# Kernel optimization log

Hardware: AMD Instinct MI355X
Metric: run time of the kernel (lower is better)

The kernel has to match this reference:

```python
import jax, jax.numpy as jnp
import numpy as np

N_NODES = 50000
N_GRAPHS = 250
NODES_PER_GRAPH = 200
EDGES_PER_GRAPH = 3200  # avg degree 16
F_IN = 128
EMB = 128
HID = 128
VOCAB = 1000
N_REL = 8


def setup_inputs() -> dict:
    key = jax.random.key(0)
    ks = jax.random.split(key, 16)

    # message: col 0 = discrete token id (stored as float), col 1 = continuous value
    disc = jax.random.randint(ks[0], (N_GRAPHS,), 0, VOCAB).astype(jnp.float32)
    cont = jax.random.normal(ks[1], (N_GRAPHS,), dtype=jnp.float32)
    message = jnp.stack([disc, cont], axis=1)  # [B, 2]

    x = jax.random.normal(ks[2], (N_NODES, F_IN), dtype=jnp.float32)

    # within-graph edges: local indices + per-graph node offset
    offs = (jnp.arange(N_GRAPHS, dtype=jnp.int64) * NODES_PER_GRAPH)[:, None]
    src = (jax.random.randint(ks[3], (N_GRAPHS, EDGES_PER_GRAPH), 0, NODES_PER_GRAPH) + offs).reshape(-1)
    dst = (jax.random.randint(ks[4], (N_GRAPHS, EDGES_PER_GRAPH), 0, NODES_PER_GRAPH) + offs).reshape(-1)
    edge_index = jnp.stack([src, dst], axis=0).astype(jnp.int64)  # [2, E]
    edge_type = jax.random.randint(ks[5], (N_GRAPHS * EDGES_PER_GRAPH,), 0, N_REL).astype(jnp.int64)

    batch = jnp.repeat(jnp.arange(N_GRAPHS, dtype=jnp.int64), NODES_PER_GRAPH)  # [N]

    s = 0.05
    W1 = jax.random.normal(ks[6], (N_REL, F_IN, EMB), dtype=jnp.float32) * s
    root1 = jax.random.normal(ks[7], (F_IN, EMB), dtype=jnp.float32) * s
    b1 = jnp.zeros((EMB,), dtype=jnp.float32)
    W2 = jax.random.normal(ks[8], (N_REL, EMB, EMB), dtype=jnp.float32) * s
    root2 = jax.random.normal(ks[9], (EMB, EMB), dtype=jnp.float32) * s
    b2 = jnp.zeros((EMB,), dtype=jnp.float32)
    embed_table = jax.random.normal(ks[10], (VOCAB, EMB), dtype=jnp.float32) * s
    cont_w = jax.random.normal(ks[11], (1, EMB), dtype=jnp.float32) * s
    cont_b = jnp.zeros((EMB,), dtype=jnp.float32)
    msg_w = jax.random.normal(ks[12], (2 * EMB, HID), dtype=jnp.float32) * s
    msg_b = jnp.zeros((HID,), dtype=jnp.float32)

    return {
        "message": message, "x": x, "edge_index": edge_index, "edge_type": edge_type,
        "batch": batch, "max_nodes": NODES_PER_GRAPH,
        "W1": W1, "root1": root1, "b1": b1, "W2": W2, "root2": root2, "b2": b2,
        "embed_table": embed_table, "cont_w": cont_w, "cont_b": cont_b,
        "msg_w": msg_w, "msg_b": msg_b,
    }


def _rgcn_conv(h, src, dst, edge_type, W, root, b, n_nodes, n_rel):
    # per-node per-relation transform, then gather per edge: avoids [E,F,F] weight gather
    hW = jnp.einsum('nf,rfo->nro', h, W)          # [N, R, O]
    msg = hW[src, edge_type]                       # [E, O]
    # mean aggregation per (dst, relation) as in PyG RGCNConv(aggr='mean')
    key_dr = dst * n_rel + edge_type
    cnt = jax.ops.segment_sum(jnp.ones_like(edge_type, dtype=h.dtype), key_dr,
                              num_segments=n_nodes * n_rel)
    norm = 1.0 / jnp.maximum(cnt[key_dr], 1.0)     # [E]
    agg = jax.ops.segment_sum(msg * norm[:, None], dst, num_segments=n_nodes)  # [N, O]
    return agg + h @ root + b


def reference(message, x, edge_index, edge_type, batch, max_nodes,
              W1, root1, b1, W2, root2, b2,
              embed_table, cont_w, cont_b, msg_w, msg_b):
    n_nodes = x.shape[0]
    n_rel = W1.shape[0]
    n_graphs = message.shape[0]
    src, dst = edge_index[0], edge_index[1]

    # --- RGCN node embeddings (2 layers, ReLU between) ---
    h = _rgcn_conv(x, src, dst, edge_type, W1, root1, b1, n_nodes, n_rel)
    h = jax.nn.relu(h)
    node_emb = _rgcn_conv(h, src, dst, edge_type, W2, root2, b2, n_nodes, n_rel)  # [N, EMB]

    # --- message representation ---
    disc_tok = message[:, 0].astype(jnp.int32)
    disc_emb = embed_table[disc_tok]                                   # [B, EMB]
    cont_emb = jax.nn.relu(message[:, 1:2] @ cont_w + cont_b)          # [B, EMB]
    combined = jnp.concatenate([disc_emb, cont_emb], axis=1)           # [B, 2*EMB]
    message_repr = jax.nn.relu(combined @ msg_w + msg_b)               # [B, HID]

    # --- per-node dot score against its graph's message, padded per graph ---
    scores = jnp.einsum('ne,ne->n', node_emb, message_repr[batch])     # [N]
    counts = jax.ops.segment_sum(jnp.ones((n_nodes,), dtype=jnp.int32), batch,
                                 num_segments=n_graphs)
    start = jnp.cumsum(counts) - counts                                # exclusive cumsum
    pos = jnp.arange(n_nodes) - start[batch]                           # slot within graph
    logits = jnp.full((n_graphs, max_nodes), -jnp.inf, dtype=scores.dtype)
    logits = logits.at[batch, pos].set(scores)
    return logits
```

## Files before the change

### kernel.cpp

```cpp
#include <hip/hip_runtime.h>
#include <stdint.h>

#define G_   250
#define P_   200
#define EPG  3200
#define E_   800000
#define F_   128
#define R_   8
#define HROW 136
#define NKEY (R_ * P_)

typedef _Float16 f16x8 __attribute__((ext_vector_type(8)));
typedef _Float16 f16x4 __attribute__((ext_vector_type(4)));
typedef float    f32x4 __attribute__((ext_vector_type(4)));

__global__ __launch_bounds__(256) void k_wstage(const float* __restrict__ W1, const float* __restrict__ root1,
                                                const float* __restrict__ W2, const float* __restrict__ root2,
                                                _Float16* __restrict__ wf) {
  int t = blockIdx.x * 256 + threadIdx.x;
  if (t >= 2 * 9 * 8 * 4 * 64 * 8) return;
  int j = t & 7;
  int rest = t >> 3;
  int lane = rest & 63; rest >>= 6;
  int kt = rest & 3;    rest >>= 2;
  int nt = rest & 7;    rest >>= 3;
  int r = rest % 9;
  int l = rest / 9;
  int k = kt * 32 + (lane >> 4) * 8 + j;
  int n = nt * 16 + (lane & 15);
  const float* Wl = (l == 0) ? W1 : W2;
  const float* rl = (l == 0) ? root1 : root2;
  float v = (r < 8) ? Wl[(r * F_ + k) * F_ + n] : rl[k * F_ + n];
  wf[t] = (_Float16)v;
}

__global__ __launch_bounds__(512, 2) void k_main(
    const float* __restrict__ x, const int* __restrict__ ei, const int* __restrict__ et,
    const _Float16* __restrict__ wf, const float* __restrict__ b1, const float* __restrict__ b2,
    const float* __restrict__ message, const float* __restrict__ embed,
    const float* __restrict__ cw, const float* __restrict__ cb,
    const float* __restrict__ mw, const float* __restrict__ mb,
    float* __restrict__ out) {
  __shared__ __attribute__((aligned(16))) _Float16 hbuf[P_ * HROW];
  __shared__ __attribute__((aligned(16))) _Float16 S[P_ * HROW];
  __shared__ int offsS[NKEY + 1];
  __shared__ unsigned short csrS[EPG];
  __shared__ float msgS[F_ + 1];
  int g = blockIdx.x, tid = threadIdx.x;
  int lane = tid & 63, wave = tid >> 6, quad = lane >> 4, lc = lane & 15;

  int*   Sint     = (int*)S;
  int*   cnt      = Sint;
  int*   cur      = Sint + 1600;
  int*   chunkTot = Sint + 3200;
  int*   scanA    = Sint + 3400;
  int*   scanB    = Sint + 3656;
  float* comb     = (float*)(Sint + 3912);
  float* red      = comb + 256;
  int*   eRec     = (int*)(red + 512);

  for (int i = tid; i < P_ * 32; i += 512) {
    int row = i >> 5, c4 = i & 31;
    const float4 v = ((const float4*)x)[(g * P_ + row) * 32 + c4];
    f16x4 pk = { (_Float16)v.x, (_Float16)v.y, (_Float16)v.z, (_Float16)v.w };
    *((f16x4*)&hbuf[row * HROW + c4 * 4]) = pk;
  }
  for (int i = tid; i < NKEY; i += 512) { cnt[i] = 0; cur[i] = 0; }
  if (tid < F_) {
    int tok = (int)message[g * 2];
    float cont = message[g * 2 + 1];
    comb[tid] = embed[tok * F_ + tid];
    float ce = cont * cw[tid] + cb[tid];
    comb[F_ + tid] = ce > 0.0f ? ce : 0.0f;
  }
  __syncthreads();
  int base = g * EPG, nbase = g * P_;
  for (int e = tid; e < EPG; e += 512) {
    int s = ei[base + e] - nbase;
    int d = ei[E_ + base + e] - nbase;
    int r = et[base + e];
    eRec[e] = s | (d << 8) | (r << 16);
    atomicAdd(&cnt[r * P_ + d], 1);
  }
  __syncthreads();
  if (tid < 200) {
    int s = 0;
    for (int i = 0; i < 8; i++) { int c = cnt[tid * 8 + i]; offsS[tid * 8 + i] = s; s += c; }
    chunkTot[tid] = s;
    scanA[tid] = s;
  }
  __syncthreads();
  {
    int* src = scanA; int* dst = scanB;
    for (int st = 1; st < 256; st <<= 1) {
      if (tid < 200) dst[tid] = src[tid] + (tid >= st ? src[tid - st] : 0);
      __syncthreads();
      int* tmp = src; src = dst; dst = tmp;
    }
  }
  if (tid < 200) {
    int add = scanA[tid] - chunkTot[tid];
    for (int i = 0; i < 8; i++) offsS[tid * 8 + i] += add;
  }
  if (tid == 0) offsS[NKEY] = EPG;
  {
    int col = tid & 127, seg = tid >> 7;
    float acc = 0.0f;
#pragma unroll 8
    for (int k = seg * 64; k < seg * 64 + 64; k++) acc += comb[k] * mw[k * F_ + col];
    red[tid] = acc;
  }
  __syncthreads();
  for (int e = tid; e < EPG; e += 512) {
    int rec = eRec[e];
    int s = rec & 255, d = (rec >> 8) & 255, r = rec >> 16;
    int key = r * P_ + d;
    int pos = atomicAdd(&cur[key], 1);
    csrS[offsS[key] + pos] = (unsigned short)s;
  }
  if (tid < F_) {
    float a = mb[tid] + red[tid] + red[128 + tid] + red[256 + tid] + red[384 + tid];
    a = a > 0.0f ? a : 0.0f;
    msgS[tid] = a;
    comb[tid] = a * b2[tid];
  }
  __syncthreads();
  if (tid < 64) comb[tid] += comb[tid + 64];
  __syncthreads();
  if (tid < 32) comb[tid] += comb[tid + 32];
  __syncthreads();
  if (tid < 16) comb[tid] += comb[tid + 16];
  __syncthreads();
  if (tid == 0) {
    float s = 0.0f;
    for (int i = 0; i < 16; i++) s += comb[i];
    msgS[F_] = s;
  }

  int mgrp = wave >> 1, ngrp = wave & 1;
  int dsub = tid >> 4;
  int c8 = (tid & 15) * 8;

  for (int l = 0; l < 2; l++) {
    f32x4 acc[4][4];
#pragma unroll
    for (int a = 0; a < 4; a++)
#pragma unroll
      for (int b = 0; b < 4; b++) acc[a][b] = f32x4{0.0f, 0.0f, 0.0f, 0.0f};
    const _Float16* wl = wf + l * (9 * 8 * 4 * 64 * 8);
    for (int r = 0; r < 9; r++) {
      __syncthreads();
      f16x8 Bf[4][4];
      const _Float16* wr = wl + r * (8 * 4 * 64 * 8);
#pragma unroll
      for (int ntj = 0; ntj < 4; ntj++)
#pragma unroll
        for (int kt = 0; kt < 4; kt++)
          Bf[ntj][kt] = *((const f16x8*)(wr + (((ngrp * 4 + ntj) * 4 + kt) * 64 + lane) * 8));
      if (r < 8) {
        int rbase = r * P_;
#pragma unroll
        for (int half = 0; half < 2; half++) {
          int d0 = half * 128 + dsub;
          int o0[4], n[4];
#pragma unroll
          for (int c = 0; c < 4; c++) {
            int d = d0 + c * 32;
            if (d < P_) { int a0 = offsS[rbase + d]; int a1 = offsS[rbase + d + 1]; o0[c] = a0; n[c] = a1 - a0; }
            else { o0[c] = 0; n[c] = 0; }
          }
          int nm = n[0];
#pragma unroll
          for (int c = 1; c < 4; c++) nm = n[c] > nm ? n[c] : nm;
          f16x8 ac[4];
#pragma unroll
          for (int c = 0; c < 4; c++) ac[c] = f16x8{0, 0, 0, 0, 0, 0, 0, 0};
          for (int t = 0; t < nm; t++) {
#pragma unroll
            for (int c = 0; c < 4; c++) {
              if (t < n[c]) {
                int s = csrS[o0[c] + t];
                ac[c] += *((const f16x8*)&hbuf[s * HROW + c8]);
              }
            }
          }
#pragma unroll
          for (int c = 0; c < 4; c++) {
            int d = d0 + c * 32;
            if (d < P_) {
              float nf = n[c] > 0 ? 1.0f / (float)n[c] : 0.0f;
              _Float16 nh = (_Float16)nf;
              f16x8 o = ac[c] * nh;
              *((f16x8*)&S[d * HROW + c8]) = o;
            }
          }
        }
      }
      __syncthreads();
      const _Float16* Ap = (r < 8) ? S : hbuf;
#pragma unroll
      for (int mtj = 0; mtj < 4; mtj++) {
        int mt = mgrp + mtj * 4;
        if (mt < 13) {
          int rowA = mt * 16 + lc; rowA = rowA < P_ ? rowA : P_ - 1;
#pragma unroll
          for (int kt = 0; kt < 4; kt++) {
            f16x8 a = *((const f16x8*)&Ap[rowA * HROW + kt * 32 + quad * 8]);
#pragma unroll
            for (int ntj = 0; ntj < 4; ntj++)
              acc[mtj][ntj] = __builtin_amdgcn_mfma_f32_16x16x32_f16(a, Bf[ntj][kt], acc[mtj][ntj], 0, 0, 0);
          }
        }
      }
    }
    __syncthreads();
    if (l == 0) {
#pragma unroll
      for (int mtj = 0; mtj < 4; mtj++) {
        int mt = mgrp + mtj * 4;
        if (mt < 13) {
#pragma unroll
          for (int ntj = 0; ntj < 4; ntj++) {
            int col = (ngrp * 4 + ntj) * 16 + lc;
            float bias = b1[col];
#pragma unroll
            for (int reg = 0; reg < 4; reg++) {
              int row = mt * 16 + quad * 4 + reg;
              float v = acc[mtj][ntj][reg] + bias;
              v = v > 0.0f ? v : 0.0f;
              if (row < P_) hbuf[row * HROW + col] = (_Float16)v;
            }
          }
        }
      }
    } else {
      float* scoreS = (float*)S;
#pragma unroll
      for (int mtj = 0; mtj < 4; mtj++) {
        int mt = mgrp + mtj * 4;
        if (mt < 13) {
#pragma unroll
          for (int reg = 0; reg < 4; reg++) {
            float p = 0.0f;
#pragma unroll
            for (int ntj = 0; ntj < 4; ntj++)
              p += acc[mtj][ntj][reg] * msgS[(ngrp * 4 + ntj) * 16 + lc];
            p += __shfl_xor(p, 8, 16);
            p += __shfl_xor(p, 4, 16);
            p += __shfl_xor(p, 2, 16);
            p += __shfl_xor(p, 1, 16);
            int row = mt * 16 + quad * 4 + reg;
            if (lc == 0 && row < P_) scoreS[ngrp * P_ + row] = p;
          }
        }
      }
      __syncthreads();
      for (int i = tid; i < P_; i += 512)
        out[g * P_ + i] = scoreS[i] + scoreS[P_ + i] + msgS[F_];
    }
  }
}

extern "C" void kernel_launch(void* const* d_in, const int* in_sizes, int n_in,
                              void* d_out, int out_size, void* d_ws, size_t ws_size,
                              hipStream_t stream) {
  const float* message = (const float*)d_in[0];
  const float* x       = (const float*)d_in[1];
  const int*   ei      = (const int*)d_in[2];
  const int*   et      = (const int*)d_in[3];
  const float* W1      = (const float*)d_in[6];
  const float* root1   = (const float*)d_in[7];
  const float* b1      = (const float*)d_in[8];
  const float* W2      = (const float*)d_in[9];
  const float* root2   = (const float*)d_in[10];
  const float* b2      = (const float*)d_in[11];
  const float* embed   = (const float*)d_in[12];
  const float* cw      = (const float*)d_in[13];
  const float* cb      = (const float*)d_in[14];
  const float* mw      = (const float*)d_in[15];
  const float* mb      = (const float*)d_in[16];

  _Float16* wfrag = (_Float16*)d_ws;
  float*    out   = (float*)d_out;

  hipLaunchKernelGGL(k_wstage, dim3(1152), dim3(256), 0, stream, W1, root1, W2, root2, wfrag);
  hipLaunchKernelGGL(k_main, dim3(G_), dim3(512), 0, stream, x, ei, et, wfrag, b1, b2,
                     message, embed, cw, cb, mw, mb, out);
}
```

Baseline: 207.1 us.

## Fuse neighbor aggregation into MFMA A-fragment loads, drop S staging buffer

Instead of first aggregating each relation's mean neighbor features into a shared S buffer and then running MFMAs from it, each wave now gathers and averages neighbor rows directly into its A fragments right before the MFMAs. This removes the S buffer writes and reads plus two barriers per relation. Because the 128-wide S buffer is gone, the scratch arrays get their own shared declarations and occupancy hint changes. The trade-off is that aggregation work is duplicated across the two n-group waves sharing an m-tile, and degree imbalance now varies per lane.

```diff
diff --git a/kernel.cpp b/kernel.cpp
--- a/kernel.cpp
+++ b/kernel.cpp
@@ -34,7 +34,7 @@
   wf[t] = (_Float16)v;
 }
 
-__global__ __launch_bounds__(512, 2) void k_main(
+__global__ __launch_bounds__(512) void k_main(
     const float* __restrict__ x, const int* __restrict__ ei, const int* __restrict__ et,
     const _Float16* __restrict__ wf, const float* __restrict__ b1, const float* __restrict__ b2,
     const float* __restrict__ message, const float* __restrict__ embed,
@@ -42,22 +42,21 @@
     const float* __restrict__ mw, const float* __restrict__ mb,
     float* __restrict__ out) {
   __shared__ __attribute__((aligned(16))) _Float16 hbuf[P_ * HROW];
-  __shared__ __attribute__((aligned(16))) _Float16 S[P_ * HROW];
+  __shared__ unsigned short csrS[EPG];
   __shared__ int offsS[NKEY + 1];
-  __shared__ unsigned short csrS[EPG];
   __shared__ float msgS[F_ + 1];
+  __shared__ float scoreS[2 * P_];
+  __shared__ int cnt[NKEY];
+  __shared__ int cur[NKEY];
+  __shared__ int chunkTot[200];
+  __shared__ int scanA[256];
+  __shared__ int scanB[256];
+  __shared__ int eRec[EPG];
+  __shared__ float comb[256];
+  __shared__ float red[512];
+
   int g = blockIdx.x, tid = threadIdx.x;
   int lane = tid & 63, wave = tid >> 6, quad = lane >> 4, lc = lane & 15;
-
-  int*   Sint     = (int*)S;
-  int*   cnt      = Sint;
-  int*   cur      = Sint + 1600;
-  int*   chunkTot = Sint + 3200;
-  int*   scanA    = Sint + 3400;
-  int*   scanB    = Sint + 3656;
-  float* comb     = (float*)(Sint + 3912);
-  float* red      = comb + 256;
-  int*   eRec     = (int*)(red + 512);
 
   for (int i = tid; i < P_ * 32; i += 512) {
     int row = i >> 5, c4 = i & 31;
@@ -136,10 +135,11 @@
     for (int i = 0; i < 16; i++) s += comb[i];
     msgS[F_] = s;
   }
+  __syncthreads();
 
   int mgrp = wave >> 1, ngrp = wave & 1;
-  int dsub = tid >> 4;
-  int c8 = (tid & 15) * 8;
+  int myD = lc;
+  int cq = quad * 8;
 
   for (int l = 0; l < 2; l++) {
     f32x4 acc[4][4];
@@ -149,7 +149,6 @@
       for (int b = 0; b < 4; b++) acc[a][b] = f32x4{0.0f, 0.0f, 0.0f, 0.0f};
     const _Float16* wl = wf + l * (9 * 8 * 4 * 64 * 8);
     for (int r = 0; r < 9; r++) {
-      __syncthreads();
       f16x8 Bf[4][4];
       const _Float16* wr = wl + r * (8 * 4 * 64 * 8);
 #pragma unroll
@@ -157,58 +156,43 @@
 #pragma unroll
         for (int kt = 0; kt < 4; kt++)
           Bf[ntj][kt] = *((const f16x8*)(wr + (((ngrp * 4 + ntj) * 4 + kt) * 64 + lane) * 8));
-      if (r < 8) {
-        int rbase = r * P_;
-#pragma unroll
-        for (int half = 0; half < 2; half++) {
-          int d0 = half * 128 + dsub;
-          int o0[4], n[4];
-#pragma unroll
-          for (int c = 0; c < 4; c++) {
-            int d = d0 + c * 32;
-            if (d < P_) { int a0 = offsS[rbase + d]; int a1 = offsS[rbase + d + 1]; o0[c] = a0; n[c] = a1 - a0; }
-            else { o0[c] = 0; n[c] = 0; }
-          }
-          int nm = n[0];
-#pragma unroll
-          for (int c = 1; c < 4; c++) nm = n[c] > nm ? n[c] : nm;
-          f16x8 ac[4];
-#pragma unroll
-          for (int c = 0; c < 4; c++) ac[c] = f16x8{0, 0, 0, 0, 0, 0, 0, 0};
-          for (int t = 0; t < nm; t++) {
-#pragma unroll
-            for (int c = 0; c < 4; c++) {
-              if (t < n[c]) {
-                int s = csrS[o0[c] + t];
-                ac[c] += *((const f16x8*)&hbuf[s * HROW + c8]);
-              }
-            }
-          }
-#pragma unroll
-          for (int c = 0; c < 4; c++) {
-            int d = d0 + c * 32;
-            if (d < P_) {
-              float nf = n[c] > 0 ? 1.0f / (float)n[c] : 0.0f;
-              _Float16 nh = (_Float16)nf;
-              f16x8 o = ac[c] * nh;
-              *((f16x8*)&S[d * HROW + c8]) = o;
-            }
-          }
-        }
-      }
-      __syncthreads();
-      const _Float16* Ap = (r < 8) ? S : hbuf;
 #pragma unroll
       for (int mtj = 0; mtj < 4; mtj++) {
         int mt = mgrp + mtj * 4;
         if (mt < 13) {
-          int rowA = mt * 16 + lc; rowA = rowA < P_ ? rowA : P_ - 1;
-#pragma unroll
-          for (int kt = 0; kt < 4; kt++) {
-            f16x8 a = *((const f16x8*)&Ap[rowA * HROW + kt * 32 + quad * 8]);
-#pragma unroll
-            for (int ntj = 0; ntj < 4; ntj++)
-              acc[mtj][ntj] = __builtin_amdgcn_mfma_f32_16x16x32_f16(a, Bf[ntj][kt], acc[mtj][ntj], 0, 0, 0);
+          f16x8 a0, a1, a2, a3;
+          if (r < 8) {
+            int d = mt * 16 + myD;
+            int o = 0, n = 0;
+            if (d < P_) { int key = r * P_ + d; o = offsS[key]; n = offsS[key + 1] - o; }
+            a0 = f16x8{0,0,0,0,0,0,0,0}; a1 = a0; a2 = a0; a3 = a0;
+            int sNext = (n > 0) ? (int)csrS[o] : 0;
+            for (int t = 0; t < n; t++) {
+              int sc = sNext;
+              if (t + 1 < n) sNext = (int)csrS[o + t + 1];
+              const _Float16* hp = &hbuf[sc * HROW + cq];
+              a0 += *((const f16x8*)(hp));
+              a1 += *((const f16x8*)(hp + 32));
+              a2 += *((const f16x8*)(hp + 64));
+              a3 += *((const f16x8*)(hp + 96));
+            }
+            float nf = (n > 0) ? 1.0f / (float)n : 0.0f;
+            _Float16 nh = (_Float16)nf;
+            a0 *= nh; a1 *= nh; a2 *= nh; a3 *= nh;
+          } else {
+            int rowA = mt * 16 + myD; rowA = rowA < P_ ? rowA : P_ - 1;
+            const _Float16* hp = &hbuf[rowA * HROW + cq];
+            a0 = *((const f16x8*)(hp));
+            a1 = *((const f16x8*)(hp + 32));
+            a2 = *((const f16x8*)(hp + 64));
+            a3 = *((const f16x8*)(hp + 96));
+          }
+#pragma unroll
+          for (int ntj = 0; ntj < 4; ntj++) {
+            acc[mtj][ntj] = __builtin_amdgcn_mfma_f32_16x16x32_f16(a0, Bf[ntj][0], acc[mtj][ntj], 0, 0, 0);
+            acc[mtj][ntj] = __builtin_amdgcn_mfma_f32_16x16x32_f16(a1, Bf[ntj][1], acc[mtj][ntj], 0, 0, 0);
+            acc[mtj][ntj] = __builtin_amdgcn_mfma_f32_16x16x32_f16(a2, Bf[ntj][2], acc[mtj][ntj], 0, 0, 0);
+            acc[mtj][ntj] = __builtin_amdgcn_mfma_f32_16x16x32_f16(a3, Bf[ntj][3], acc[mtj][ntj], 0, 0, 0);
           }
         }
       }
@@ -233,8 +217,8 @@
           }
         }
       }
+      __syncthreads();
     } else {
-      float* scoreS = (float*)S;
 #pragma unroll
       for (int mtj = 0; mtj < 4; mtj++) {
         int mt = mgrp + mtj * 4;
```

Result: faster. 189.2 us (-8.7%).
